# Performance work log

Measured on AMD Instinct MI355X. Metric: run time of the kernel, lower is better.

The kernel has to match this reference:

```python
import jax, jax.numpy as jnp
import numpy as np


def setup_inputs() -> dict:
    key = jax.random.key(0)
    ks = jax.random.split(key, 5)
    N, T, d, H, O = 64, 512, 512, 1024, 1

    def xavier(k, shape):
        fan_in, fan_out = shape[1], shape[0]
        limit = float(np.sqrt(6.0 / (fan_in + fan_out)))
        return jax.random.uniform(k, shape, jnp.float32, -limit, limit)

    return {
        "x": jax.random.normal(ks[0], (N, T, d), jnp.float32),
        "w_ih": xavier(ks[1], (4 * H, d)),
        "w_hh": xavier(ks[2], (4 * H, H)),
        "b_ih": jnp.zeros((4 * H,), jnp.float32),
        "b_hh": jnp.zeros((4 * H,), jnp.float32),
        "fc_w": xavier(ks[3], (O, H)),
        "fc_b": jnp.zeros((O,), jnp.float32),
    }


def reference(x, w_ih, w_hh, b_ih, b_hh, fc_w, fc_b):
    N, T, d = x.shape
    H = w_hh.shape[1]

    # Precompute input projections for all timesteps in one big GEMM: (N,T,4H)
    x_proj = jnp.einsum("ntd,gd->ntg", x, w_ih) + b_ih + b_hh

    def step(carry, xp_t):
        h, c = carry
        gates = xp_t + h @ w_hh.T  # (N, 4H)
        i, f, g, o = jnp.split(gates, 4, axis=-1)  # torch LSTMCell order: i,f,g,o
        i = jax.nn.sigmoid(i)
        f = jax.nn.sigmoid(f)
        g = jnp.tanh(g)
        o = jax.nn.sigmoid(o)
        c_new = f * c + i * g
        h_new = o * jnp.tanh(c_new)
        return (h_new, c_new), None

    h0 = jnp.zeros((N, H), x.dtype)
    c0 = jnp.zeros((N, H), x.dtype)
    (h_T, _), _ = jax.lax.scan(step, (h0, c0), jnp.swapaxes(x_proj, 0, 1))

    y = h_T @ fc_w.T + fc_b
    return jax.nn.sigmoid(y)
```

## Files before the change

kernel.cpp:

```cpp
#include <hip/hip_runtime.h>
#include <hip/hip_bf16.h>

typedef __bf16 bf16x8 __attribute__((ext_vector_type(8)));
typedef float f32x4 __attribute__((ext_vector_type(4)));
typedef unsigned int u32x4 __attribute__((ext_vector_type(4)));
typedef unsigned short u16;
typedef unsigned int u32;

__device__ __forceinline__ u16 f2bf(float f) {
  union { float f; unsigned int i; } c;
  c.f = f;
  unsigned int x = c.i;
  return (u16)((x + 0x7fffu + ((x >> 16) & 1u)) >> 16);
}
__device__ __forceinline__ float sigm(float x) { return 1.f / (1.f + __expf(-x)); }
__device__ __forceinline__ float tanh_fast(float x) {
  float e2 = __expf(2.f * x);
  return 1.f - 2.f / (e2 + 1.f);
}

__global__ void cvt_f32_bf16_v4(const float* __restrict__ in, u16* __restrict__ out, int n4) {
  int stride = gridDim.x * blockDim.x;
  for (int i = blockIdx.x * blockDim.x + threadIdx.x; i < n4; i += stride) {
    float4 v = reinterpret_cast<const float4*>(in)[i];
    union { u16 u[4]; uint2 d; } o;
    o.u[0] = f2bf(v.x); o.u[1] = f2bf(v.y); o.u[2] = f2bf(v.z); o.u[3] = f2bf(v.w);
    reinterpret_cast<uint2*>(out)[i] = o.d;
  }
}

__global__ void cvt_x_transpose(const float* __restrict__ in, u16* __restrict__ out,
                                u32* __restrict__ hbuf_u) {
  int gid = blockIdx.x * blockDim.x + threadIdx.x;
  if (gid < 65536) hbuf_u[gid] = ((gid >> 13) & 1) ? 1u : 0u;
  if (gid >= 64 * 512 * 64) return;
  int k8 = gid & 63, t = (gid >> 6) & 511, n = gid >> 15;
  const float* src = in + ((size_t)(n * 512 + t) << 9) + (k8 << 3);
  float4 a = reinterpret_cast<const float4*>(src)[0];
  float4 b = reinterpret_cast<const float4*>(src)[1];
  union { u16 u[8]; uint4 d; } o;
  o.u[0] = f2bf(a.x); o.u[1] = f2bf(a.y); o.u[2] = f2bf(a.z); o.u[3] = f2bf(a.w);
  o.u[4] = f2bf(b.x); o.u[5] = f2bf(b.y); o.u[6] = f2bf(b.z); o.u[7] = f2bf(b.w);
  *reinterpret_cast<uint4*>(out + ((size_t)(t * 64 + n) << 9) + (k8 << 3)) = o.d;
}

__global__ void __launch_bounds__(256, 1) lstm_seq(
    const u16* __restrict__ xb,
    const u16* __restrict__ wib,
    const float* __restrict__ w_hh,
    u32* __restrict__ hbuf_u,
    float* __restrict__ hTf,
    const float* __restrict__ b_ih, const float* __restrict__ b_hh) {
  __shared__ u16 wh[64][1032];
  __shared__ float gp[4][16][68];

  int blk = blockIdx.x, t = threadIdx.x;
  int grp = blk & 3, sli = blk >> 2;
  int u0 = sli << 4;

  for (int idx = t; idx < 64 * 128; idx += 256) {
    int l = idx >> 7, c8 = idx & 127;
    int gr = ((l >> 4) << 10) + u0 + (l & 15);
    const float* src = w_hh + ((size_t)gr << 10) + c8 * 8;
    float4 a = reinterpret_cast<const float4*>(src)[0];
    float4 c = reinterpret_cast<const float4*>(src)[1];
    union { u16 us[8]; bf16x8 v; } o;
    o.us[0] = f2bf(a.x); o.us[1] = f2bf(a.y); o.us[2] = f2bf(a.z); o.us[3] = f2bf(a.w);
    o.us[4] = f2bf(c.x); o.us[5] = f2bf(c.y); o.us[6] = f2bf(c.z); o.us[7] = f2bf(c.w);
    *(bf16x8*)(&wh[l][c8 * 8]) = o.v;
  }

  int lane = t & 63, wv = t >> 6;
  int lr = lane & 15, hi = lane >> 4, lk8 = hi << 3;

  int prow = t >> 4, pul = t & 15;
  float bI = b_ih[u0 + pul]        + b_hh[u0 + pul];
  float bF = b_ih[1024 + u0 + pul] + b_hh[1024 + u0 + pul];
  float bG = b_ih[2048 + u0 + pul] + b_hh[2048 + u0 + pul];
  float bO = b_ih[3072 + u0 + pul] + b_hh[3072 + u0 + pul];
  float c_ = 0.f;

  u32* hgrp = hbuf_u + (grp << 14);
  __syncthreads();

  for (int s = 0; s < 512; ++s) {
    f32x4 acc[4] = {};

    {
      const u16* xb_ = xb + ((size_t)s << 15) + (size_t)(((grp << 4) + lr) << 9) + (wv << 7) + lk8;
      const u16* wb_ = wib + ((size_t)(u0 + lr) << 9) + (wv << 7) + lk8;
#pragma unroll
      for (int ks = 0; ks < 4; ++ks) {
        bf16x8 a = *(const bf16x8*)(xb_ + ks * 32);
#pragma unroll
        for (int nt = 0; nt < 4; ++nt) {
          bf16x8 bfr = *(const bf16x8*)(wb_ + ((size_t)nt << 19) + ks * 32);
          acc[nt] = __builtin_amdgcn_mfma_f32_16x16x32_bf16(a, bfr, acc[nt], 0, 0, 0);
        }
      }
    }

    if (s > 0) {
      const u32* hb4 = hgrp + ((s & 1) << 13) + (lr << 9) + (wv << 7) + (hi << 2);
      u32 par = (u32)((s >> 1) & 1);
      u32x4 ha[8];
      int tries = 0;
      while (true) {
#define LDH(OFF) asm volatile("global_load_dwordx4 %0, %1, off offset:" #OFF " sc0 sc1" \
                              : "=v"(ha[OFF / 64]) : "v"(hb4) : "memory");
        LDH(0) LDH(64) LDH(128) LDH(192) LDH(256) LDH(320) LDH(384) LDH(448)
#undef LDH
        asm volatile("s_waitcnt vmcnt(0)" ::: "memory");
        __builtin_amdgcn_sched_barrier(0);
        u32 ok;
        if (par) {
          u32 r = 0xFFFFFFFFu;
#pragma unroll
          for (int i2 = 0; i2 < 8; ++i2)
            r &= (ha[i2][0] & ha[i2][1]) & (ha[i2][2] & ha[i2][3]);
          ok = r & 1u;
        } else {
          u32 r = 0u;
#pragma unroll
          for (int i2 = 0; i2 < 8; ++i2)
            r |= (ha[i2][0] | ha[i2][1]) | (ha[i2][2] | ha[i2][3]);
          ok = (~r) & 1u;
        }
        if (__all((int)ok)) break;
        if (++tries > (1 << 20)) break;
        __builtin_amdgcn_s_sleep(1);
      }
      __builtin_amdgcn_sched_barrier(0);
#pragma unroll
      for (int ks = 0; ks < 8; ++ks) {
        union { u32x4 uu; bf16x8 v; } af; af.uu = ha[ks];
#pragma unroll
        for (int nt = 0; nt < 4; ++nt) {
          bf16x8 bfr = *(const bf16x8*)(&wh[(nt << 4) + lr][(wv << 8) + ks * 32 + lk8]);
          acc[nt] = __builtin_amdgcn_mfma_f32_16x16x32_bf16(af.v, bfr, acc[nt], 0, 0, 0);
        }
      }
    }

#pragma unroll
    for (int nt = 0; nt < 4; ++nt)
#pragma unroll
      for (int q = 0; q < 4; ++q)
        gp[wv][(hi << 2) + q][(nt << 4) + lr] = acc[nt][q];
    __syncthreads();

    float g0 = gp[0][prow][pul]      + gp[1][prow][pul]      + gp[2][prow][pul]      + gp[3][prow][pul]      + bI;
    float g1 = gp[0][prow][16 + pul] + gp[1][prow][16 + pul] + gp[2][prow][16 + pul] + gp[3][prow][16 + pul] + bF;
    float g2 = gp[0][prow][32 + pul] + gp[1][prow][32 + pul] + gp[2][prow][32 + pul] + gp[3][prow][32 + pul] + bG;
    float g3 = gp[0][prow][48 + pul] + gp[1][prow][48 + pul] + gp[2][prow][48 + pul] + gp[3][prow][48 + pul] + bO;
    float ii = sigm(g0), ff = sigm(g1), tg = tanh_fast(g2), oo = sigm(g3);
    float cn = ff * c_ + ii * tg;
    c_ = cn;
    float hv = oo * tanh_fast(cn);
    if (s == 511) {
      hTf[((size_t)((grp << 4) + prow) << 10) + u0 + pul] = hv;
    } else {
      u32 hb = (u32)f2bf(hv);
      u32 pn = (u32)__shfl_xor((int)hb, 1, 64);
      if (!(pul & 1)) {
        u32 par1 = (u32)(((s + 1) >> 1) & 1);
        u32 wdat = ((hb & ~1u) | par1) | (pn << 16);
        u32* dst = hgrp + (((s + 1) & 1) << 13) + (prow << 9) + (sli << 3) + (pul >> 1);
        asm volatile("global_store_dword %0, %1, off sc0 sc1" :: "v"(dst), "v"(wdat) : "memory");
      }
    }
    __syncthreads();
  }
}

__global__ void fc_head(const float* __restrict__ hTf, const float* __restrict__ fc_w,
                        const float* __restrict__ fc_b, float* __restrict__ out) {
  __shared__ float red[4];
  int n = blockIdx.x, t = threadIdx.x;
  float4 hv = *(const float4*)(hTf + (n << 10) + t * 4);
  float4 wv = *(const float4*)(fc_w + t * 4);
  float s = hv.x * wv.x + hv.y * wv.y + hv.z * wv.z + hv.w * wv.w;
#pragma unroll
  for (int o = 32; o; o >>= 1) s += __shfl_down(s, o, 64);
  if ((t & 63) == 0) red[t >> 6] = s;
  __syncthreads();
  if (t == 0) out[n] = sigm(red[0] + red[1] + red[2] + red[3] + fc_b[0]);
}

extern "C" void kernel_launch(void* const* d_in, const int* in_sizes, int n_in,
                              void* d_out, int out_size, void* d_ws, size_t ws_size,
                              hipStream_t stream) {
  const float* x    = (const float*)d_in[0];
  const float* w_ih = (const float*)d_in[1];
  const float* w_hh = (const float*)d_in[2];
  const float* b_ih = (const float*)d_in[3];
  const float* b_hh = (const float*)d_in[4];
  const float* fc_w = (const float*)d_in[5];
  const float* fc_b = (const float*)d_in[6];
  float* out = (float*)d_out;

  char* ws = (char*)d_ws;
  u16*   xb     = (u16*)(ws);
  u16*   wib    = (u16*)(ws + 33554432);
  u32*   hbuf_u = (u32*)(ws + 37748736);
  float* hTf    = (float*)(ws + 38010880);

  cvt_x_transpose<<<8192, 256, 0, stream>>>(x, xb, hbuf_u);
  cvt_f32_bf16_v4<<<512, 256, 0, stream>>>(w_ih, wib, 2097152 / 4);
  lstm_seq<<<256, 256, 0, stream>>>(xb, wib, w_hh, hbuf_u, hTf, b_ih, b_hh);
  fc_head<<<64, 256, 0, stream>>>(hTf, fc_w, fc_b, out);
}
```

Baseline: 1.528 ms.

## Hoist W_ih fragments into registers, transpose gate scratch, batch h stores as dwordx4

The W_ih bf16 fragments each wave needs are loaded into registers once before the time loop, so they are no longer re-fetched from global memory every step. The gate partial-sum scratch is transposed to [4][64][17] to change its LDS bank access pattern. The per-thread dword h publishes are staged in LDS and then written by 32 threads as dwordx4 stores, which cuts the number of global store transactions on the inter-block sync path. This costs 64 extra VGPRs per thread for the cached weights, and the h store now happens after the barrier. The parity flag is still encoded per dword, so polling readers should not see torn updates.

```diff
diff --git a/kernel.cpp b/kernel.cpp
--- a/kernel.cpp
+++ b/kernel.cpp
@@ -52,7 +52,8 @@
     float* __restrict__ hTf,
     const float* __restrict__ b_ih, const float* __restrict__ b_hh) {
   __shared__ u16 wh[64][1032];
-  __shared__ float gp[4][16][68];
+  __shared__ float gp[4][64][17];
+  __shared__ __align__(16) u32 hstg[16][8];
 
   int blk = blockIdx.x, t = threadIdx.x;
   int grp = blk & 3, sli = blk >> 2;
@@ -72,14 +73,24 @@
 
   int lane = t & 63, wv = t >> 6;
   int lr = lane & 15, hi = lane >> 4, lk8 = hi << 3;
-
   int prow = t >> 4, pul = t & 15;
+
   float bI = b_ih[u0 + pul]        + b_hh[u0 + pul];
   float bF = b_ih[1024 + u0 + pul] + b_hh[1024 + u0 + pul];
   float bG = b_ih[2048 + u0 + pul] + b_hh[2048 + u0 + pul];
   float bO = b_ih[3072 + u0 + pul] + b_hh[3072 + u0 + pul];
   float c_ = 0.f;
 
+  bf16x8 wi_r[4][4];
+  {
+    const u16* wb_ = wib + ((size_t)(u0 + lr) << 9) + (wv << 7) + lk8;
+#pragma unroll
+    for (int nt = 0; nt < 4; ++nt)
+#pragma unroll
+      for (int ks = 0; ks < 4; ++ks)
+        wi_r[nt][ks] = *(const bf16x8*)(wb_ + ((size_t)nt << 19) + ks * 32);
+  }
+
   u32* hgrp = hbuf_u + (grp << 14);
   __syncthreads();
 
@@ -88,15 +99,12 @@
 
     {
       const u16* xb_ = xb + ((size_t)s << 15) + (size_t)(((grp << 4) + lr) << 9) + (wv << 7) + lk8;
-      const u16* wb_ = wib + ((size_t)(u0 + lr) << 9) + (wv << 7) + lk8;
 #pragma unroll
       for (int ks = 0; ks < 4; ++ks) {
         bf16x8 a = *(const bf16x8*)(xb_ + ks * 32);
 #pragma unroll
-        for (int nt = 0; nt < 4; ++nt) {
-          bf16x8 bfr = *(const bf16x8*)(wb_ + ((size_t)nt << 19) + ks * 32);
-          acc[nt] = __builtin_amdgcn_mfma_f32_16x16x32_bf16(a, bfr, acc[nt], 0, 0, 0);
-        }
+        for (int nt = 0; nt < 4; ++nt)
+          acc[nt] = __builtin_amdgcn_mfma_f32_16x16x32_bf16(a, wi_r[nt][ks], acc[nt], 0, 0, 0);
       }
     }
 
@@ -146,17 +154,18 @@
     for (int nt = 0; nt < 4; ++nt)
 #pragma unroll
       for (int q = 0; q < 4; ++q)
-        gp[wv][(hi << 2) + q][(nt << 4) + lr] = acc[nt][q];
+        gp[wv][(nt << 4) + lr][(hi << 2) + q] = acc[nt][q];
     __syncthreads();
 
-    float g0 = gp[0][prow][pul]      + gp[1][prow][pul]      + gp[2][prow][pul]      + gp[3][prow][pul]      + bI;
-    float g1 = gp[0][prow][16 + pul] + gp[1][prow][16 + pul] + gp[2][prow][16 + pul] + gp[3][prow][16 + pul] + bF;
-    float g2 = gp[0][prow][32 + pul] + gp[1][prow][32 + pul] + gp[2][prow][32 + pul] + gp[3][prow][32 + pul] + bG;
-    float g3 = gp[0][prow][48 + pul] + gp[1][prow][48 + pul] + gp[2][prow][48 + pul] + gp[3][prow][48 + pul] + bO;
+    float g0 = gp[0][pul][prow]      + gp[1][pul][prow]      + gp[2][pul][prow]      + gp[3][pul][prow]      + bI;
+    float g1 = gp[0][16 + pul][prow] + gp[1][16 + pul][prow] + gp[2][16 + pul][prow] + gp[3][16 + pul][prow] + bF;
+    float g2 = gp[0][32 + pul][prow] + gp[1][32 + pul][prow] + gp[2][32 + pul][prow] + gp[3][32 + pul][prow] + bG;
+    float g3 = gp[0][48 + pul][prow] + gp[1][48 + pul][prow] + gp[2][48 + pul][prow] + gp[3][48 + pul][prow] + bO;
     float ii = sigm(g0), ff = sigm(g1), tg = tanh_fast(g2), oo = sigm(g3);
     float cn = ff * c_ + ii * tg;
     c_ = cn;
     float hv = oo * tanh_fast(cn);
+
     if (s == 511) {
       hTf[((size_t)((grp << 4) + prow) << 10) + u0 + pul] = hv;
     } else {
@@ -164,12 +173,17 @@
       u32 pn = (u32)__shfl_xor((int)hb, 1, 64);
       if (!(pul & 1)) {
         u32 par1 = (u32)(((s + 1) >> 1) & 1);
-        u32 wdat = ((hb & ~1u) | par1) | (pn << 16);
-        u32* dst = hgrp + (((s + 1) & 1) << 13) + (prow << 9) + (sli << 3) + (pul >> 1);
-        asm volatile("global_store_dword %0, %1, off sc0 sc1" :: "v"(dst), "v"(wdat) : "memory");
+        hstg[prow][pul >> 1] = ((hb & ~1u) | par1) | (pn << 16);
       }
     }
     __syncthreads();
+
+    if (s < 511 && t < 32) {
+      int row = t >> 1, part = t & 1;
+      u32x4 v = *(const u32x4*)(&hstg[row][part << 2]);
+      u32* dst = hgrp + (((s + 1) & 1) << 13) + (row << 9) + (sli << 3) + (part << 2);
+      asm volatile("global_store_dwordx4 %0, %1, off sc0 sc1" :: "v"(dst), "v"(v) : "memory");
+    }
   }
 }
 
```

Measured after the change: 1.543 ms. Within noise of the previous version (+1.0%).

## Quantize recurrent weights and hidden state to int8 with per-row scales

Applied to the files above, without the earlier changes.

Replaces the bf16 recurrent GEMM with int8 MFMA (16x16x64), quantizing W_hh per row with a scale held in LDS and the hidden state with a fixed 127 scale. Blocks are regrouped to 8 batch groups by 32 units, so each block handles 8 rows and 128 gate columns. The exchanged h buffer is halved to bytes, and the spin loop first polls without sc1 and skips the sleep. This cuts the per-step global traffic and the MFMA work on the serial critical path, but int8 quantization of h and W_hh loses accuracy. Half of each 16-row MFMA tile is wasted because only 8 rows are valid.

```diff
diff --git a/kernel.cpp b/kernel.cpp
--- a/kernel.cpp
+++ b/kernel.cpp
@@ -3,9 +3,11 @@
 
 typedef __bf16 bf16x8 __attribute__((ext_vector_type(8)));
 typedef float f32x4 __attribute__((ext_vector_type(4)));
+typedef int   i32x4 __attribute__((ext_vector_type(4)));
 typedef unsigned int u32x4 __attribute__((ext_vector_type(4)));
 typedef unsigned short u16;
 typedef unsigned int u32;
+typedef unsigned char u8;
 
 __device__ __forceinline__ u16 f2bf(float f) {
   union { float f; unsigned int i; } c;
@@ -30,9 +32,9 @@
 }
 
 __global__ void cvt_x_transpose(const float* __restrict__ in, u16* __restrict__ out,
-                                u32* __restrict__ hbuf_u) {
+                                u32* __restrict__ hring_u) {
   int gid = blockIdx.x * blockDim.x + threadIdx.x;
-  if (gid < 65536) hbuf_u[gid] = ((gid >> 13) & 1) ? 1u : 0u;
+  if (gid < 32768) hring_u[gid] = ((gid >> 11) & 1) ? 1u : 0u;
   if (gid >= 64 * 512 * 64) return;
   int k8 = gid & 63, t = (gid >> 6) & 511, n = gid >> 15;
   const float* src = in + ((size_t)(n * 512 + t) << 9) + (k8 << 3);
@@ -48,128 +50,165 @@
     const u16* __restrict__ xb,
     const u16* __restrict__ wib,
     const float* __restrict__ w_hh,
-    u32* __restrict__ hbuf_u,
+    u8* __restrict__ hring,
     float* __restrict__ hTf,
     const float* __restrict__ b_ih, const float* __restrict__ b_hh) {
-  __shared__ u16 wh[64][1032];
-  __shared__ float gp[4][16][68];
+  __shared__ u8 wh[128][1056];
+  __shared__ float gp[4][8][132];
+  __shared__ float invs[128];
+  __shared__ float rmax[128][2];
+  __shared__ u8 hstg8[8][32];
 
   int blk = blockIdx.x, t = threadIdx.x;
-  int grp = blk & 3, sli = blk >> 2;
-  int u0 = sli << 4;
-
-  for (int idx = t; idx < 64 * 128; idx += 256) {
-    int l = idx >> 7, c8 = idx & 127;
-    int gr = ((l >> 4) << 10) + u0 + (l & 15);
-    const float* src = w_hh + ((size_t)gr << 10) + c8 * 8;
-    float4 a = reinterpret_cast<const float4*>(src)[0];
-    float4 c = reinterpret_cast<const float4*>(src)[1];
-    union { u16 us[8]; bf16x8 v; } o;
-    o.us[0] = f2bf(a.x); o.us[1] = f2bf(a.y); o.us[2] = f2bf(a.z); o.us[3] = f2bf(a.w);
-    o.us[4] = f2bf(c.x); o.us[5] = f2bf(c.y); o.us[6] = f2bf(c.z); o.us[7] = f2bf(c.w);
-    *(bf16x8*)(&wh[l][c8 * 8]) = o.v;
+  int grp = blk & 7, sli = blk >> 3;
+  int u0 = sli << 5;
+
+  {
+    int l = t >> 1, hf = t & 1;
+    int gr = ((l >> 5) << 10) + u0 + (l & 31);
+    const float* src = w_hh + ((size_t)gr << 10) + (hf << 9);
+    float mx = 0.f;
+    for (int c = 0; c < 128; ++c) {
+      float4 v = reinterpret_cast<const float4*>(src)[c];
+      mx = fmaxf(mx, fmaxf(fmaxf(fabsf(v.x), fabsf(v.y)), fmaxf(fabsf(v.z), fabsf(v.w))));
+    }
+    rmax[l][hf] = mx;
+    __syncthreads();
+    float m = fmaxf(rmax[l][0], rmax[l][1]);
+    float q = m > 0.f ? 127.f / m : 0.f;
+    if (hf == 0) invs[l] = m / (127.f * 127.f);
+    for (int c = 0; c < 128; ++c) {
+      float4 v = reinterpret_cast<const float4*>(src)[c];
+      u32 b0 = (u32)(u8)(char)__float2int_rn(v.x * q);
+      u32 b1 = (u32)(u8)(char)__float2int_rn(v.y * q);
+      u32 b2 = (u32)(u8)(char)__float2int_rn(v.z * q);
+      u32 b3 = (u32)(u8)(char)__float2int_rn(v.w * q);
+      *(u32*)&wh[l][(hf << 9) + (c << 2)] = b0 | (b1 << 8) | (b2 << 16) | (b3 << 24);
+    }
   }
 
   int lane = t & 63, wv = t >> 6;
-  int lr = lane & 15, hi = lane >> 4, lk8 = hi << 3;
-
-  int prow = t >> 4, pul = t & 15;
-  float bI = b_ih[u0 + pul]        + b_hh[u0 + pul];
-  float bF = b_ih[1024 + u0 + pul] + b_hh[1024 + u0 + pul];
-  float bG = b_ih[2048 + u0 + pul] + b_hh[2048 + u0 + pul];
-  float bO = b_ih[3072 + u0 + pul] + b_hh[3072 + u0 + pul];
+  int lr = lane & 15, hi = lane >> 4, row8 = lane & 7;
+
+  int pr = t >> 5, pu = t & 31;
+  float bI = b_ih[u0 + pu]        + b_hh[u0 + pu];
+  float bF = b_ih[1024 + u0 + pu] + b_hh[1024 + u0 + pu];
+  float bG = b_ih[2048 + u0 + pu] + b_hh[2048 + u0 + pu];
+  float bO = b_ih[3072 + u0 + pu] + b_hh[3072 + u0 + pu];
   float c_ = 0.f;
 
-  u32* hgrp = hbuf_u + (grp << 14);
+  u8* hring_g = hring + (grp << 14);
   __syncthreads();
 
   for (int s = 0; s < 512; ++s) {
-    f32x4 acc[4] = {};
+    f32x4 accf[8] = {};
+    i32x4 acci[8] = {};
 
     {
-      const u16* xb_ = xb + ((size_t)s << 15) + (size_t)(((grp << 4) + lr) << 9) + (wv << 7) + lk8;
-      const u16* wb_ = wib + ((size_t)(u0 + lr) << 9) + (wv << 7) + lk8;
+      const u16* xrow = xb + ((size_t)s << 15) + (((grp << 3) + row8) << 9) + (wv << 7) + (hi << 3);
 #pragma unroll
       for (int ks = 0; ks < 4; ++ks) {
-        bf16x8 a = *(const bf16x8*)(xb_ + ks * 32);
-#pragma unroll
-        for (int nt = 0; nt < 4; ++nt) {
-          bf16x8 bfr = *(const bf16x8*)(wb_ + ((size_t)nt << 19) + ks * 32);
-          acc[nt] = __builtin_amdgcn_mfma_f32_16x16x32_bf16(a, bfr, acc[nt], 0, 0, 0);
+        bf16x8 a = *(const bf16x8*)(xrow + ks * 32);
+#pragma unroll
+        for (int nt = 0; nt < 8; ++nt) {
+          int col = (nt << 4) + lr;
+          int grow = ((col >> 5) << 10) + u0 + (col & 31);
+          bf16x8 bfr = *(const bf16x8*)(wib + ((size_t)grow << 9) + (wv << 7) + (ks << 5) + (hi << 3));
+          accf[nt] = __builtin_amdgcn_mfma_f32_16x16x32_bf16(a, bfr, accf[nt], 0, 0, 0);
         }
       }
     }
 
     if (s > 0) {
-      const u32* hb4 = hgrp + ((s & 1) << 13) + (lr << 9) + (wv << 7) + (hi << 2);
+      const u8* hb = hring_g + ((s & 1) << 13) + (row8 << 10) + (wv << 8) + (hi << 4);
       u32 par = (u32)((s >> 1) & 1);
-      u32x4 ha[8];
+      u32x4 ha[4];
       int tries = 0;
       while (true) {
-#define LDH(OFF) asm volatile("global_load_dwordx4 %0, %1, off offset:" #OFF " sc0 sc1" \
-                              : "=v"(ha[OFF / 64]) : "v"(hb4) : "memory");
-        LDH(0) LDH(64) LDH(128) LDH(192) LDH(256) LDH(320) LDH(384) LDH(448)
-#undef LDH
+        if (tries < 6) {
+          asm volatile(
+            "global_load_dwordx4 %0, %4, off offset:0 sc0\n\t"
+            "global_load_dwordx4 %1, %4, off offset:64 sc0\n\t"
+            "global_load_dwordx4 %2, %4, off offset:128 sc0\n\t"
+            "global_load_dwordx4 %3, %4, off offset:192 sc0"
+            : "=v"(ha[0]), "=v"(ha[1]), "=v"(ha[2]), "=v"(ha[3])
+            : "v"(hb) : "memory");
+        } else {
+          asm volatile(
+            "global_load_dwordx4 %0, %4, off offset:0 sc0 sc1\n\t"
+            "global_load_dwordx4 %1, %4, off offset:64 sc0 sc1\n\t"
+            "global_load_dwordx4 %2, %4, off offset:128 sc0 sc1\n\t"
+            "global_load_dwordx4 %3, %4, off offset:192 sc0 sc1"
+            : "=v"(ha[0]), "=v"(ha[1]), "=v"(ha[2]), "=v"(ha[3])
+            : "v"(hb) : "memory");
+        }
         asm volatile("s_waitcnt vmcnt(0)" ::: "memory");
         __builtin_amdgcn_sched_barrier(0);
         u32 ok;
         if (par) {
           u32 r = 0xFFFFFFFFu;
 #pragma unroll
-          for (int i2 = 0; i2 < 8; ++i2)
+          for (int i2 = 0; i2 < 4; ++i2)
             r &= (ha[i2][0] & ha[i2][1]) & (ha[i2][2] & ha[i2][3]);
           ok = r & 1u;
         } else {
           u32 r = 0u;
 #pragma unroll
-          for (int i2 = 0; i2 < 8; ++i2)
+          for (int i2 = 0; i2 < 4; ++i2)
             r |= (ha[i2][0] | ha[i2][1]) | (ha[i2][2] | ha[i2][3]);
           ok = (~r) & 1u;
         }
         if (__all((int)ok)) break;
         if (++tries > (1 << 20)) break;
-        __builtin_amdgcn_s_sleep(1);
+        if (tries > 6) __builtin_amdgcn_s_sleep(1);
       }
       __builtin_amdgcn_sched_barrier(0);
 #pragma unroll
-      for (int ks = 0; ks < 8; ++ks) {
-        union { u32x4 uu; bf16x8 v; } af; af.uu = ha[ks];
-#pragma unroll
-        for (int nt = 0; nt < 4; ++nt) {
-          bf16x8 bfr = *(const bf16x8*)(&wh[(nt << 4) + lr][(wv << 8) + ks * 32 + lk8]);
-          acc[nt] = __builtin_amdgcn_mfma_f32_16x16x32_bf16(af.v, bfr, acc[nt], 0, 0, 0);
-        }
-      }
-    }
-
-#pragma unroll
-    for (int nt = 0; nt < 4; ++nt)
-#pragma unroll
-      for (int q = 0; q < 4; ++q)
-        gp[wv][(hi << 2) + q][(nt << 4) + lr] = acc[nt][q];
+      for (int kk = 0; kk < 4; ++kk) {
+        union { u32x4 u; i32x4 v; } av; av.u = ha[kk];
+#pragma unroll
+        for (int nt = 0; nt < 8; ++nt) {
+          i32x4 bv = *(const i32x4*)&wh[(nt << 4) + lr][(wv << 8) + (kk << 6) + (hi << 4)];
+          acci[nt] = __builtin_amdgcn_mfma_i32_16x16x64_i8(av.v, bv, acci[nt], 0, 0, 0);
+        }
+      }
+    }
+
+    if (hi < 2) {
+#pragma unroll
+      for (int nt = 0; nt < 8; ++nt) {
+        float iv = invs[(nt << 4) + lr];
+#pragma unroll
+        for (int q = 0; q < 4; ++q)
+          gp[wv][(hi << 2) + q][(nt << 4) + lr] = accf[nt][q] + (float)acci[nt][q] * iv;
+      }
+    }
     __syncthreads();
 
-    float g0 = gp[0][prow][pul]      + gp[1][prow][pul]      + gp[2][prow][pul]      + gp[3][prow][pul]      + bI;
-    float g1 = gp[0][prow][16 + pul] + gp[1][prow][16 + pul] + gp[2][prow][16 + pul] + gp[3][prow][16 + pul] + bF;
-    float g2 = gp[0][prow][32 + pul] + gp[1][prow][32 + pul] + gp[2][prow][32 + pul] + gp[3][prow][32 + pul] + bG;
-    float g3 = gp[0][prow][48 + pul] + gp[1][prow][48 + pul] + gp[2][prow][48 + pul] + gp[3][prow][48 + pul] + bO;
-    float ii = sigm(g0), ff = sigm(g1), tg = tanh_fast(g2), oo = sigm(g3);
-    float cn = ff * c_ + ii * tg;
-    c_ = cn;
-    float hv = oo * tanh_fast(cn);
-    if (s == 511) {
-      hTf[((size_t)((grp << 4) + prow) << 10) + u0 + pul] = hv;
-    } else {
-      u32 hb = (u32)f2bf(hv);
-      u32 pn = (u32)__shfl_xor((int)hb, 1, 64);
-      if (!(pul & 1)) {
-        u32 par1 = (u32)(((s + 1) >> 1) & 1);
-        u32 wdat = ((hb & ~1u) | par1) | (pn << 16);
-        u32* dst = hgrp + (((s + 1) & 1) << 13) + (prow << 9) + (sli << 3) + (pul >> 1);
-        asm volatile("global_store_dword %0, %1, off sc0 sc1" :: "v"(dst), "v"(wdat) : "memory");
+    {
+      float g0 = gp[0][pr][pu]      + gp[1][pr][pu]      + gp[2][pr][pu]      + gp[3][pr][pu]      + bI;
+      float g1 = gp[0][pr][32 + pu] + gp[1][pr][32 + pu] + gp[2][pr][32 + pu] + gp[3][pr][32 + pu] + bF;
+      float g2 = gp[0][pr][64 + pu] + gp[1][pr][64 + pu] + gp[2][pr][64 + pu] + gp[3][pr][64 + pu] + bG;
+      float g3 = gp[0][pr][96 + pu] + gp[1][pr][96 + pu] + gp[2][pr][96 + pu] + gp[3][pr][96 + pu] + bO;
+      float ii = sigm(g0), ff = sigm(g1), tg = tanh_fast(g2), oo = sigm(g3);
+      float cn = ff * c_ + ii * tg;
+      c_ = cn;
+      float hv = oo * tanh_fast(cn);
+      if (s == 511) {
+        hTf[(((size_t)(grp << 3) + pr) << 10) + u0 + pu] = hv;
+      } else {
+        hstg8[pr][pu] = (u8)(char)__float2int_rn(hv * 127.f);
       }
     }
     __syncthreads();
+
+    if (s < 511 && t < 64) {
+      int r = t >> 3, j = t & 7;
+      u32 w = *(const u32*)&hstg8[r][j << 2];
+      w = (w & ~1u) | (u32)(((s + 1) >> 1) & 1);
+      u8* dst = hring_g + (((s + 1) & 1) << 13) + (r << 10) + u0 + (j << 2);
+      asm volatile("global_store_dword %0, %1, off sc0 sc1" :: "v"(dst), "v"(w) : "memory");
+    }
   }
 }
 
@@ -200,13 +239,13 @@
   float* out = (float*)d_out;
 
   char* ws = (char*)d_ws;
-  u16*   xb     = (u16*)(ws);
-  u16*   wib    = (u16*)(ws + 33554432);
-  u32*   hbuf_u = (u32*)(ws + 37748736);
-  float* hTf    = (float*)(ws + 38010880);
-
-  cvt_x_transpose<<<8192, 256, 0, stream>>>(x, xb, hbuf_u);
+  u16*   xb    = (u16*)(ws);
+  u16*   wib   = (u16*)(ws + 33554432);
+  u8*    hring = (u8*)(ws + 37748736);
+  float* hTf   = (float*)(ws + 37879808);
+
+  cvt_x_transpose<<<8192, 256, 0, stream>>>(x, xb, (u32*)hring);
   cvt_f32_bf16_v4<<<512, 256, 0, stream>>>(w_ih, wib, 2097152 / 4);
-  lstm_seq<<<256, 256, 0, stream>>>(xb, wib, w_hh, hbuf_u, hTf, b_ih, b_hh);
+  lstm_seq<<<256, 256, 0, stream>>>(xb, wib, w_hh, hring, hTf, b_ih, b_hh);
   fc_head<<<64, 256, 0, stream>>>(hTf, fc_w, fc_b, out);
 }
```

Result: slower. 2.046 ms (+33.9%).
